# Kernel tuning notes

Hardware: AMD Instinct MI355X
Metric: run time of the kernel (lower is better)

## Reference

```python
import jax, jax.numpy as jnp
import numpy as np

REG_C = 0.01
REG_THETA_M = 0.01
REG_THETA_P = 0.01
EPS = 1e-20


def setup_inputs() -> dict:
    key = jax.random.key(0)
    k1, k2, k3 = jax.random.split(key, 3)
    B, L, M, P = 128, 16, 32, 4  # batch, num_site, M, P
    input_ds = jax.random.uniform(k1, (B, L), dtype=jnp.float32)
    theta = jax.random.uniform(k2, (L, M, P), dtype=jnp.float32, minval=-1.0, maxval=1.0)
    coef = jax.random.uniform(k3, (M, P), dtype=jnp.float32, minval=-1.0, maxval=1.0)
    return {"input_ds": input_ds, "theta": theta, "coef": coef}


def reference(input_ds, theta, coef):
    # theta: (L, M, P); coef: (M, P); input_ds: (B, L)
    L, M, P = theta.shape
    p_range = jnp.arange(P, dtype=theta.dtype)
    scaling_factor = jnp.pi / 2.0 ** (p_range + 1.0)          # (P,)
    x = scaling_factor[None, None, :] * input_ds[:, :, None]   # (B, L, P)

    # prob term: sum_{m,p} coef[m,p] * prod_l cos(theta[l,m,p] + x[b,l,p])
    theta_x = theta[None, :, :, :] + x[:, :, None, :]          # (B, L, M, P)
    amp = jnp.einsum('bmp,mp->b', jnp.prod(jnp.cos(theta_x), axis=1), coef)
    prob = amp ** 2                                            # (B,)

    # normalization term over the big (B, L, M, M, P, P) broadcast tensor
    d_theta = theta[:, :, None, :, None] - theta[:, None, :, None, :]   # (L, M, M, P, P)
    d_x = x[:, :, None, None, :, None] - x[:, :, None, None, None, :]   # (B, L, 1, 1, P, P)
    cos_prod = jnp.prod(jnp.cos(d_theta[None] + d_x), axis=1)           # (B, M, M, P, P)
    coef_tensor = jnp.einsum('mp,nq->mnpq', coef, coef)                 # (M, M, P, P)
    normalization = jnp.einsum('bmnpq,mnpq->b', cos_prod, coef_tensor)  # (B,)

    prob_norm = prob / normalization

    # regularization (torch.var is unbiased -> ddof=1)
    reg_theta_m = jnp.mean(jnp.var(theta, axis=1, ddof=1))
    reg_theta_p = jnp.mean(jnp.var(theta, axis=2, ddof=1)) if P != 1 else 0.0
    reg_c = jnp.var(coef, ddof=1)

    loss = (jnp.mean(-jnp.log(prob_norm + EPS))
            + REG_C * reg_c
            + REG_THETA_M * reg_theta_m
            + REG_THETA_P * reg_theta_p)
    return loss
```

## Files before the change

### kernel.cpp

```cpp
#include <hip/hip_runtime.h>
#include <math.h>

#define NB 128
#define NL 16
#define NM 32
#define NP 4
#define NMP 128

__global__ __launch_bounds__(512) void per_b_kernel(
    const float* __restrict__ ds, const float* __restrict__ theta,
    const float* __restrict__ coef, float* __restrict__ wnorm,
    float* __restrict__ wamp)
{
    const int b    = blockIdx.x >> 1;
    const int h    = blockIdx.x & 1;
    const int t    = threadIdx.x;
    const int lane = t & 63;
    const int w    = t >> 6;

    __shared__ float2 cs[NL][NMP];
    __shared__ float  co[NMP];
    __shared__ float  dsrow[NL];
    __shared__ float  redN[8], redA[8];

    if (t < NL)  dsrow[t] = ds[b * NL + t];
    if (t < NMP) co[t]    = coef[t];
    __syncthreads();

    for (int i = t; i < NL * NMP; i += 512) {
        int l = i >> 7;
        int j = i & (NMP - 1);
        int p = j & 3;
        float sf = (float)M_PI / (float)(2 << p);
        float u  = theta[i] + sf * dsrow[l];
        float ss, cc;
        __sincosf(u, &ss, &cc);
        cs[l][j] = make_float2(cc, ss);
    }
    __syncthreads();

    float rc0[NL], rs0[NL], rc1[NL], rs1[NL];
    #pragma unroll
    for (int l = 0; l < NL; ++l) {
        float2 v0 = cs[l][lane];      rc0[l] = v0.x; rs0[l] = v0.y;
        float2 v1 = cs[l][lane + 64]; rc1[l] = v1.x; rs1[l] = v1.y;
    }
    const float wj0 = co[lane], wj1 = co[lane + 64];

    float amp_part = 0.f;
    if (w == 0) {
        float p0 = wj0, p1 = wj1;
        #pragma unroll
        for (int l = 0; l < NL; ++l) { p0 *= rc0[l]; p1 *= rc1[l]; }
        amp_part = p0 + p1;
    }

    float norm_part = 0.f;
    const int k0 = h * 64 + w * 8;
    #pragma unroll 4
    for (int ki = 0; ki < 8; ++ki) {
        int k = k0 + ki;
        float pp0 = 1.f, pp1 = 1.f;
        #pragma unroll
        for (int l = 0; l < NL; ++l) {
            float2 v = cs[l][k];
            pp0 *= fmaf(rc0[l], v.x, rs0[l] * v.y);
            pp1 *= fmaf(rc1[l], v.x, rs1[l] * v.y);
        }
        norm_part = fmaf(fmaf(wj1, pp1, wj0 * pp0), co[k], norm_part);
    }

    #pragma unroll
    for (int off = 32; off > 0; off >>= 1) {
        norm_part += __shfl_xor(norm_part, off);
        amp_part  += __shfl_xor(amp_part,  off);
    }
    if (lane == 0) { redN[w] = norm_part; redA[w] = amp_part; }
    __syncthreads();
    if (t == 0) {
        float n = 0.f, a = 0.f;
        #pragma unroll
        for (int i = 0; i < 8; ++i) { n += redN[i]; a += redA[i]; }
        wnorm[b * 2 + h] = n;
        if (h == 0) wamp[b] = a;
    }
}

__global__ __launch_bounds__(512) void finalize_kernel(
    const float* __restrict__ wnorm, const float* __restrict__ wamp,
    const float* __restrict__ theta, const float* __restrict__ coef,
    float* __restrict__ out)
{
    const int t    = threadIdx.x;
    const int lane = t & 63;
    const int w    = t >> 6;
    __shared__ float r5[5][8];

    float mnl = 0.f;
    if (t < NB) {
        float a = wamp[t];
        float n = wnorm[2 * t] + wnorm[2 * t + 1];
        mnl = -__logf(a * a / n + 1e-20f);
    }
    float cv = (t < NMP) ? coef[t] : 0.f;

    float vm = 0.f;
    if (t < NL * NP) {
        int l = t >> 2, p = t & 3;
        float sum = 0.f, sum2 = 0.f;
        for (int m = 0; m < NM; ++m) {
            float x = theta[(l * NM + m) * NP + p];
            sum += x; sum2 += x * x;
        }
        vm = (sum2 - sum * sum / (float)NM) / (float)(NM - 1);
    }

    float4 th = reinterpret_cast<const float4*>(theta)[t];
    float sum  = th.x + th.y + th.z + th.w;
    float sum2 = th.x * th.x + th.y * th.y + th.z * th.z + th.w * th.w;
    float vp = (sum2 - sum * sum * 0.25f) * (1.f / 3.f);

    float v1 = mnl, v2 = cv, v3 = cv * cv, v4 = vm, v5 = vp;
    #pragma unroll
    for (int off = 32; off > 0; off >>= 1) {
        v1 += __shfl_xor(v1, off);
        v2 += __shfl_xor(v2, off);
        v3 += __shfl_xor(v3, off);
        v4 += __shfl_xor(v4, off);
        v5 += __shfl_xor(v5, off);
    }
    if (lane == 0) {
        r5[0][w] = v1; r5[1][w] = v2; r5[2][w] = v3; r5[3][w] = v4; r5[4][w] = v5;
    }
    __syncthreads();
    if (t == 0) {
        float s1 = 0.f, s2 = 0.f, s3 = 0.f, s4 = 0.f, s5 = 0.f;
        #pragma unroll
        for (int i = 0; i < 8; ++i) {
            s1 += r5[0][i]; s2 += r5[1][i]; s3 += r5[2][i];
            s4 += r5[3][i]; s5 += r5[4][i];
        }
        float s_mnl  = s1 / (float)NB;
        float reg_c  = (s3 - s2 * s2 / (float)NMP) / (float)(NMP - 1);
        float reg_tm = s4 / (float)(NL * NP);
        float reg_tp = s5 / (float)(NL * NM);
        out[0] = s_mnl + 0.01f * (reg_c + reg_tm + reg_tp);
    }
}

extern "C" void kernel_launch(void* const* d_in, const int* in_sizes, int n_in,
                              void* d_out, int out_size, void* d_ws, size_t ws_size,
                              hipStream_t stream) {
    const float* ds    = (const float*)d_in[0];
    const float* theta = (const float*)d_in[1];
    const float* coef  = (const float*)d_in[2];
    float* wnorm = (float*)d_ws;
    float* wamp  = (float*)d_ws + 2 * NB;
    float* out   = (float*)d_out;

    per_b_kernel<<<2 * NB, 512, 0, stream>>>(ds, theta, coef, wnorm, wamp);
    finalize_kernel<<<1, 512, 0, stream>>>(wnorm, wamp, theta, coef, out);
}
```

Before: 12.79 us.

## Fuse per-batch and finalize kernels into one with atomic accumulation

Merges the two-kernel pipeline into a single kernel with one 1024-thread block per batch element, each thread handling one j column instead of two. Each block computes its own -log term and atomically adds it to the output. Block 0 also computes the regularization terms. This removes the second kernel launch and the workspace round trip, but adds a memset, a float atomic reduction with order-dependent summation, and larger blocks with fewer registers per thread.

New measurement: 18.27 us. +42.8%, slower.

```diff
diff --git a/kernel.cpp b/kernel.cpp
--- a/kernel.cpp
+++ b/kernel.cpp
@@ -7,13 +7,11 @@
 #define NP 4
 #define NMP 128
 
-__global__ __launch_bounds__(512) void per_b_kernel(
+__global__ __launch_bounds__(1024) void fused_kernel(
     const float* __restrict__ ds, const float* __restrict__ theta,
-    const float* __restrict__ coef, float* __restrict__ wnorm,
-    float* __restrict__ wamp)
+    const float* __restrict__ coef, float* __restrict__ out)
 {
-    const int b    = blockIdx.x >> 1;
-    const int h    = blockIdx.x & 1;
+    const int b    = blockIdx.x;
     const int t    = threadIdx.x;
     const int lane = t & 63;
     const int w    = t >> 6;
@@ -21,13 +19,15 @@
     __shared__ float2 cs[NL][NMP];
     __shared__ float  co[NMP];
     __shared__ float  dsrow[NL];
-    __shared__ float  redN[8], redA[8];
+    __shared__ float  redN[16], redA[16];
+    __shared__ float  r5[4][16];
 
     if (t < NL)  dsrow[t] = ds[b * NL + t];
     if (t < NMP) co[t]    = coef[t];
     __syncthreads();
 
-    for (int i = t; i < NL * NMP; i += 512) {
+    #pragma unroll
+    for (int i = t; i < NL * NMP; i += 1024) {
         int l = i >> 7;
         int j = i & (NMP - 1);
         int p = j & 3;
@@ -39,35 +39,32 @@
     }
     __syncthreads();
 
-    float rc0[NL], rs0[NL], rc1[NL], rs1[NL];
+    const int j = t & (NMP - 1);
+    float rc[NL], rs[NL];
     #pragma unroll
-    for (int l = 0; l < NL; ++l) {
-        float2 v0 = cs[l][lane];      rc0[l] = v0.x; rs0[l] = v0.y;
-        float2 v1 = cs[l][lane + 64]; rc1[l] = v1.x; rs1[l] = v1.y;
-    }
-    const float wj0 = co[lane], wj1 = co[lane + 64];
+    for (int l = 0; l < NL; ++l) { float2 v = cs[l][j]; rc[l] = v.x; rs[l] = v.y; }
+    const float wj = co[j];
 
     float amp_part = 0.f;
-    if (w == 0) {
-        float p0 = wj0, p1 = wj1;
+    if (w < 2) {
+        float p0 = wj;
         #pragma unroll
-        for (int l = 0; l < NL; ++l) { p0 *= rc0[l]; p1 *= rc1[l]; }
-        amp_part = p0 + p1;
+        for (int l = 0; l < NL; ++l) p0 *= rc[l];
+        amp_part = p0;
     }
 
     float norm_part = 0.f;
-    const int k0 = h * 64 + w * 8;
+    const int k0 = (t >> 7) * 16;
     #pragma unroll 4
-    for (int ki = 0; ki < 8; ++ki) {
+    for (int ki = 0; ki < 16; ++ki) {
         int k = k0 + ki;
-        float pp0 = 1.f, pp1 = 1.f;
+        float pp = 1.f;
         #pragma unroll
         for (int l = 0; l < NL; ++l) {
             float2 v = cs[l][k];
-            pp0 *= fmaf(rc0[l], v.x, rs0[l] * v.y);
-            pp1 *= fmaf(rc1[l], v.x, rs1[l] * v.y);
+            pp *= fmaf(rc[l], v.x, rs[l] * v.y);
         }
-        norm_part = fmaf(fmaf(wj1, pp1, wj0 * pp0), co[k], norm_part);
+        norm_part = fmaf(wj * pp, co[k], norm_part);
     }
 
     #pragma unroll
@@ -76,75 +73,53 @@
         amp_part  += __shfl_xor(amp_part,  off);
     }
     if (lane == 0) { redN[w] = norm_part; redA[w] = amp_part; }
+
+    if (b == 0) {
+        float cv = (t < NMP) ? co[t] : 0.f;
+        float v2 = cv, v3 = cv * cv, v4 = 0.f, v5 = 0.f;
+        if (t < NL * NP) {
+            int l = t >> 2, p = t & 3;
+            float sum = 0.f, sum2 = 0.f;
+            for (int m = 0; m < NM; ++m) {
+                float x = theta[(l * NM + m) * NP + p];
+                sum += x; sum2 += x * x;
+            }
+            v4 = (sum2 - sum * sum / (float)NM) / (float)(NM - 1);
+        }
+        if (t < NL * NM) {
+            float4 th = reinterpret_cast<const float4*>(theta)[t];
+            float sum  = th.x + th.y + th.z + th.w;
+            float sum2 = th.x * th.x + th.y * th.y + th.z * th.z + th.w * th.w;
+            v5 = (sum2 - sum * sum * 0.25f) * (1.f / 3.f);
+        }
+        #pragma unroll
+        for (int off = 32; off > 0; off >>= 1) {
+            v2 += __shfl_xor(v2, off);
+            v3 += __shfl_xor(v3, off);
+            v4 += __shfl_xor(v4, off);
+            v5 += __shfl_xor(v5, off);
+        }
+        if (lane == 0) { r5[0][w] = v2; r5[1][w] = v3; r5[2][w] = v4; r5[3][w] = v5; }
+    }
     __syncthreads();
+
     if (t == 0) {
         float n = 0.f, a = 0.f;
         #pragma unroll
-        for (int i = 0; i < 8; ++i) { n += redN[i]; a += redA[i]; }
-        wnorm[b * 2 + h] = n;
-        if (h == 0) wamp[b] = a;
-    }
-}
-
-__global__ __launch_bounds__(512) void finalize_kernel(
-    const float* __restrict__ wnorm, const float* __restrict__ wamp,
-    const float* __restrict__ theta, const float* __restrict__ coef,
-    float* __restrict__ out)
-{
-    const int t    = threadIdx.x;
-    const int lane = t & 63;
-    const int w    = t >> 6;
-    __shared__ float r5[5][8];
-
-    float mnl = 0.f;
-    if (t < NB) {
-        float a = wamp[t];
-        float n = wnorm[2 * t] + wnorm[2 * t + 1];
-        mnl = -__logf(a * a / n + 1e-20f);
-    }
-    float cv = (t < NMP) ? coef[t] : 0.f;
-
-    float vm = 0.f;
-    if (t < NL * NP) {
-        int l = t >> 2, p = t & 3;
-        float sum = 0.f, sum2 = 0.f;
-        for (int m = 0; m < NM; ++m) {
-            float x = theta[(l * NM + m) * NP + p];
-            sum += x; sum2 += x * x;
+        for (int i = 0; i < 16; ++i) { n += redN[i]; a += redA[i]; }
+        float val = -__logf(a * a / n + 1e-20f) * (1.f / (float)NB);
+        if (b == 0) {
+            float s2 = 0.f, s3 = 0.f, s4 = 0.f, s5 = 0.f;
+            #pragma unroll
+            for (int i = 0; i < 16; ++i) {
+                s2 += r5[0][i]; s3 += r5[1][i]; s4 += r5[2][i]; s5 += r5[3][i];
+            }
+            float reg_c  = (s3 - s2 * s2 / (float)NMP) / (float)(NMP - 1);
+            float reg_tm = s4 / (float)(NL * NP);
+            float reg_tp = s5 / (float)(NL * NM);
+            val += 0.01f * (reg_c + reg_tm + reg_tp);
         }
-        vm = (sum2 - sum * sum / (float)NM) / (float)(NM - 1);
-    }
-
-    float4 th = reinterpret_cast<const float4*>(theta)[t];
-    float sum  = th.x + th.y + th.z + th.w;
-    float sum2 = th.x * th.x + th.y * th.y + th.z * th.z + th.w * th.w;
-    float vp = (sum2 - sum * sum * 0.25f) * (1.f / 3.f);
-
-    float v1 = mnl, v2 = cv, v3 = cv * cv, v4 = vm, v5 = vp;
-    #pragma unroll
-    for (int off = 32; off > 0; off >>= 1) {
-        v1 += __shfl_xor(v1, off);
-        v2 += __shfl_xor(v2, off);
-        v3 += __shfl_xor(v3, off);
-        v4 += __shfl_xor(v4, off);
-        v5 += __shfl_xor(v5, off);
-    }
-    if (lane == 0) {
-        r5[0][w] = v1; r5[1][w] = v2; r5[2][w] = v3; r5[3][w] = v4; r5[4][w] = v5;
-    }
-    __syncthreads();
-    if (t == 0) {
-        float s1 = 0.f, s2 = 0.f, s3 = 0.f, s4 = 0.f, s5 = 0.f;
-        #pragma unroll
-        for (int i = 0; i < 8; ++i) {
-            s1 += r5[0][i]; s2 += r5[1][i]; s3 += r5[2][i];
-            s4 += r5[3][i]; s5 += r5[4][i];
-        }
-        float s_mnl  = s1 / (float)NB;
-        float reg_c  = (s3 - s2 * s2 / (float)NMP) / (float)(NMP - 1);
-        float reg_tm = s4 / (float)(NL * NP);
-        float reg_tp = s5 / (float)(NL * NM);
-        out[0] = s_mnl + 0.01f * (reg_c + reg_tm + reg_tp);
+        atomicAdd(out, val);
     }
 }
 
@@ -154,10 +129,8 @@
     const float* ds    = (const float*)d_in[0];
     const float* theta = (const float*)d_in[1];
     const float* coef  = (const float*)d_in[2];
-    float* wnorm = (float*)d_ws;
-    float* wamp  = (float*)d_ws + 2 * NB;
-    float* out   = (float*)d_out;
+    float* out = (float*)d_out;
 
-    per_b_kernel<<<2 * NB, 512, 0, stream>>>(ds, theta, coef, wnorm, wamp);
-    finalize_kernel<<<1, 512, 0, stream>>>(wnorm, wamp, theta, coef, out);
+    hipMemsetAsync(out, 0, sizeof(float), stream);
+    fused_kernel<<<NB, 1024, 0, stream>>>(ds, theta, coef, out);
 }
```
